# Kernel tuning notes

Hardware: AMD Instinct MI355X
Metric: run time of the kernel (lower is better)

Reference implementation:

```python
import jax, jax.numpy as jnp
import numpy as np

ALPHA = 0.2  # LeakyReLU negative slope

def setup_inputs() -> dict:
    key = jax.random.key(0)
    kx, kw, kb, ka = jax.random.split(key, 4)
    B, K, D, H = 4, 256, 128, 4
    x = jax.random.normal(kx, (B, K, D), dtype=jnp.float32)
    # Per-head Linear(2D -> D): stored as (H, 2D, D), i.e. transposed torch layout (y = v @ W + b)
    W = jax.random.normal(kw, (H, 2 * D, D), dtype=jnp.float32) * (1.0 / np.sqrt(2 * D))
    lin_b = jax.random.normal(kb, (H, D), dtype=jnp.float32) * 0.01
    # Per-head attention vector a: (H, D)
    a = jax.random.normal(ka, (H, D), dtype=jnp.float32) * (1.0 / np.sqrt(D))
    # Per-head additive bias over attention logits, initialized to zeros like the torch module
    bias = jnp.zeros((H, K, K), dtype=jnp.float32)
    return {"x": x, "W": W, "lin_b": lin_b, "a": a, "bias": bias}

def reference(x, W, lin_b, a, bias):
    # GATv2, dense all-pairs attention over K nodes, eval mode (dropout off).
    # Faithful decomposition: Linear(concat(x_i, x_j)) == x_i @ W_src + x_j @ W_dst + b
    B, K, D = x.shape
    H = W.shape[0]
    outs = []
    for h in range(H):  # small fixed head count; each head has distinct params
        W_src, W_dst = W[h, :D], W[h, D:]          # (D, D) each
        left = x @ W_src                            # (B, K, D) -> contribution of node i
        right = x @ W_dst                           # (B, K, D) -> contribution of node j
        s = left[:, :, None, :] + right[:, None, :, :] + lin_b[h]  # (B, K, K, D)
        s = jnp.where(s > 0, s, ALPHA * s)          # LeakyReLU
        e = jnp.einsum('bijd,d->bij', s, a[h]) + bias[h]           # (B, K, K)
        attn = jax.nn.softmax(e, axis=2)
        outs.append(attn @ x)                       # (B, K, D)
    return jnp.mean(jnp.stack(outs, axis=-1), axis=-1)
```

## Files before the change

### kernel.cpp

```cpp
#include <hip/hip_runtime.h>
#include <math.h>

constexpr int Kc = 256, Dc = 128, Mc = 1024;

typedef _Float16 h2_t __attribute__((ext_vector_type(2)));
union U32H2 { unsigned int u; h2_t h; };
__device__ inline h2_t u2h(unsigned int u) { U32H2 x; x.u = u; return x.h; }
__device__ inline unsigned int h2u(h2_t h) { U32H2 x; x.h = h; return x.u; }
__device__ inline unsigned int packh(float a, float b) {
    h2_t h; h.x = (_Float16)a; h.y = (_Float16)b; return h2u(h);
}

#if __has_builtin(__builtin_amdgcn_fdot2)
__device__ inline float dot2h(unsigned int a, unsigned int b, float c) {
    return __builtin_amdgcn_fdot2(u2h(a), u2h(b), c, false);
}
#else
__device__ inline float dot2h(unsigned int a, unsigned int b, float c) {
    h2_t ah = u2h(a), bh = u2h(b);
    return fmaf((float)ah.x, (float)bh.x, fmaf((float)ah.y, (float)bh.y, c));
}
#endif

__device__ inline float estep(unsigned int r, unsigned int l, h2_t av, float acc) {
    h2_t s = u2h(r) + u2h(l);
    unsigned int t = h2u(s) & 0x7FFF7FFFu;
#if __has_builtin(__builtin_amdgcn_fdot2)
    return __builtin_amdgcn_fdot2(u2h(t), av, acc, false);
#else
    h2_t th = u2h(t);
    return fmaf((float)th.x, (float)av.x, fmaf((float)th.y, (float)av.y, acc));
#endif
}

__global__ __launch_bounds__(512) void k1(const float* __restrict__ x,
                                          const float* __restrict__ W,
                                          const float* __restrict__ lin_b,
                                          const float* __restrict__ a,
                                          unsigned int* __restrict__ Lpp,
                                          unsigned int* __restrict__ Rtp,
                                          float* __restrict__ eb) {
    __shared__ unsigned int As2[64 * 64];
    __shared__ unsigned int Bs2[64 * 64];
    __shared__ float red[8][16][4];

    const int tid = threadIdx.x;
    const int bid = blockIdx.x;
    const int tx = tid & 15, ty = tid >> 4;
    const bool isL = (bid < 128);

    int h, b, m0, n0, dt;
    if (isL) {
        const int nt = bid & 1, mt = (bid >> 1) & 15;
        h = (bid >> 5) & 3; b = 0; dt = 0;
        m0 = mt * 64; n0 = nt * 64;
        {
            const int m_l = tid & 63, kq = tid >> 6;
            #pragma unroll
            for (int c = 0; c < 4; ++c) {
                const float4 v = *(const float4*)&x[(m0 + m_l) * Dc + kq * 16 + c * 4];
                As2[(kq * 8 + c * 2 + 0) * 64 + m_l] = packh(v.x, v.y);
                As2[(kq * 8 + c * 2 + 1) * 64 + m_l] = packh(v.z, v.w);
            }
        }
        {
            const int n_l = tid & 63, kq = tid >> 6;
            const float* Wb = W + (h * 2) * Dc * Dc;
            #pragma unroll
            for (int kk = 0; kk < 8; ++kk) {
                const int k2 = kq * 8 + kk;
                Bs2[k2 * 64 + n_l] =
                    packh(Wb[(2 * k2) * Dc + n0 + n_l], Wb[(2 * k2 + 1) * Dc + n0 + n_l]);
            }
        }
    } else {
        const int r_ = bid - 128;
        const int jt = r_ & 3;
        dt = (r_ >> 2) & 1;
        b  = (r_ >> 3) & 3;
        h  = (r_ >> 5) & 3;
        m0 = dt * 64;
        n0 = jt * 64;
        {
            const int d_l = tid & 63, kq = tid >> 6;
            const float* Wb = W + ((h * 2 + 1) * Dc) * Dc;
            #pragma unroll
            for (int kk = 0; kk < 8; ++kk) {
                const int k2 = kq * 8 + kk;
                As2[k2 * 64 + d_l] =
                    packh(Wb[(2 * k2) * Dc + m0 + d_l], Wb[(2 * k2 + 1) * Dc + m0 + d_l]);
            }
        }
        {
            const int j_l = tid & 63, kq = tid >> 6;
            #pragma unroll
            for (int c = 0; c < 4; ++c) {
                const float4 v = *(const float4*)&x[(b * Kc + n0 + j_l) * Dc + kq * 16 + c * 4];
                Bs2[(kq * 8 + c * 2 + 0) * 64 + j_l] = packh(v.x, v.y);
                Bs2[(kq * 8 + c * 2 + 1) * 64 + j_l] = packh(v.z, v.w);
            }
        }
    }
    __syncthreads();

    float acc[2][4];
    #pragma unroll
    for (int r = 0; r < 2; ++r)
        #pragma unroll
        for (int c = 0; c < 4; ++c) acc[r][c] = 0.f;

    #pragma unroll 8
    for (int k2 = 0; k2 < 64; ++k2) {
        const uint2 xa = *(const uint2*)&As2[k2 * 64 + ty * 2];
        const uint4 wb = *(const uint4*)&Bs2[k2 * 64 + tx * 4];
        acc[0][0] = dot2h(xa.x, wb.x, acc[0][0]);
        acc[0][1] = dot2h(xa.x, wb.y, acc[0][1]);
        acc[0][2] = dot2h(xa.x, wb.z, acc[0][2]);
        acc[0][3] = dot2h(xa.x, wb.w, acc[0][3]);
        acc[1][0] = dot2h(xa.y, wb.x, acc[1][0]);
        acc[1][1] = dot2h(xa.y, wb.y, acc[1][1]);
        acc[1][2] = dot2h(xa.y, wb.z, acc[1][2]);
        acc[1][3] = dot2h(xa.y, wb.w, acc[1][3]);
    }

    if (isL) {
        const float4 lv = *(const float4*)&lin_b[h * Dc + n0 + tx * 4];
        #pragma unroll
        for (int r = 0; r < 2; ++r) {
            uint2 pk;
            pk.x = packh(acc[r][0] + lv.x, acc[r][1] + lv.y);
            pk.y = packh(acc[r][2] + lv.z, acc[r][3] + lv.w);
            *(uint2*)&Lpp[(h * Mc + m0 + ty * 2 + r) * 64 + (n0 >> 1) + tx * 2] = pk;
        }
    } else {
        {
            uint4 pk;
            pk.x = packh(acc[0][0], acc[1][0]);
            pk.y = packh(acc[0][1], acc[1][1]);
            pk.z = packh(acc[0][2], acc[1][2]);
            pk.w = packh(acc[0][3], acc[1][3]);
            *(uint4*)&Rtp[((h * 4 + b) * 64 + (m0 >> 1) + ty) * Kc + n0 + tx * 4] = pk;
        }
        const float2 av = *(const float2*)&a[h * Dc + m0 + ty * 2];
        float p0 = 0.4f * (av.x * acc[0][0] + av.y * acc[1][0]);
        float p1 = 0.4f * (av.x * acc[0][1] + av.y * acc[1][1]);
        float p2 = 0.4f * (av.x * acc[0][2] + av.y * acc[1][2]);
        float p3 = 0.4f * (av.x * acc[0][3] + av.y * acc[1][3]);
        p0 += __shfl_xor(p0, 16, 64); p0 += __shfl_xor(p0, 32, 64);
        p1 += __shfl_xor(p1, 16, 64); p1 += __shfl_xor(p1, 32, 64);
        p2 += __shfl_xor(p2, 16, 64); p2 += __shfl_xor(p2, 32, 64);
        p3 += __shfl_xor(p3, 16, 64); p3 += __shfl_xor(p3, 32, 64);
        if (((tid >> 4) & 3) == 0) {
            const int w = tid >> 6;
            red[w][tx][0] = p0; red[w][tx][1] = p1;
            red[w][tx][2] = p2; red[w][tx][3] = p3;
        }
        __syncthreads();
        if (tid < 64) {
            const int txl = tid >> 2, c = tid & 3;
            float v = 0.f;
            #pragma unroll
            for (int w8 = 0; w8 < 8; ++w8) v += red[w8][txl][c];
            eb[((h * 4 + b) * 2 + dt) * Kc + n0 + tid] = 1.5f * v;
        }
    }
}

#define E4(ACC, LPV)                               \
    ACC.x = estep(rr.x, LPV, av, ACC.x);           \
    ACC.y = estep(rr.y, LPV, av, ACC.y);           \
    ACC.z = estep(rr.z, LPV, av, ACC.z);           \
    ACC.w = estep(rr.w, LPV, av, ACC.w);

__global__ __launch_bounds__(256) void k2(const float* __restrict__ x,
                                          const float* __restrict__ a,
                                          const float* __restrict__ bias,
                                          const unsigned int* __restrict__ Lpp,
                                          const unsigned int* __restrict__ Rtp,
                                          const float* __restrict__ eb,
                                          float* __restrict__ out) {
    __shared__ float red[256 * 12];
    __shared__ unsigned int lpT2[4 * 64 * 2];
    __shared__ unsigned int aa2s[4 * 64];
    __shared__ float plbar[2 * Kc];

    const int tid = threadIdx.x;
    const int L = blockIdx.x;
    const int xcd = L & 7;
    const int b = xcd >> 1;
    const int it = ((L >> 3) << 1) | (xcd & 1);
    const int i0 = it * 2;

    {
        const int hs = tid >> 6, dp = tid & 63;
        uint2 v;
        v.x = Lpp[(hs * Mc + b * Kc + i0 + 0) * 64 + dp];
        v.y = Lpp[(hs * Mc + b * Kc + i0 + 1) * 64 + dp];
        *(uint2*)&lpT2[(hs * 64 + dp) * 2] = v;
        aa2s[tid] = packh(0.4f * a[hs * Dc + 2 * dp], 0.4f * a[hs * Dc + 2 * dp + 1]);
    }
    __syncthreads();

    const int h = tid >> 6, j4 = tid & 63;
    const int hb = h * 4 + b;

    const float4 ebv0 = *(const float4*)&eb[(hb * 2 + 0) * Kc + j4 * 4];
    const float4 ebv1 = *(const float4*)&eb[(hb * 2 + 1) * Kc + j4 * 4];
    const float4 bv0  = *(const float4*)&bias[(h * Kc + i0 + 0) * Kc + j4 * 4];
    const float4 bv1  = *(const float4*)&bias[(h * Kc + i0 + 1) * Kc + j4 * 4];

    float4 acc0 = make_float4(0.f, 0.f, 0.f, 0.f);
    float4 acc1 = make_float4(0.f, 0.f, 0.f, 0.f);
    {
        const unsigned int* rb = Rtp + (hb * 64) * Kc + j4 * 4;
        const unsigned int* lt = lpT2 + (h * 64) * 2;
        const unsigned int* at = aa2s + h * 64;

        uint4 cur[8], nxt[8];
        #pragma unroll
        for (int i = 0; i < 8; ++i) cur[i] = *(const uint4*)(rb + i * Kc);

        #pragma unroll
        for (int bb = 0; bb < 8; ++bb) {
            #pragma unroll
            for (int i = 0; i < 8; ++i)
                if (bb < 7) nxt[i] = *(const uint4*)(rb + ((bb + 1) * 8 + i) * Kc);
            #pragma unroll
            for (int i = 0; i < 8; ++i) {
                const int dp = bb * 8 + i;
                const uint4 rr = cur[i];
                const uint2 lp2 = *(const uint2*)(lt + dp * 2);
                const h2_t av = u2h(at[dp]);
                E4(acc0, lp2.x);
                E4(acc1, lp2.y);
            }
            #pragma unroll
            for (int i = 0; i < 8; ++i)
                if (bb < 7) cur[i] = nxt[i];
        }
    }

    {
        const float jx = ebv0.x + ebv1.x, jy = ebv0.y + ebv1.y;
        const float jz = ebv0.z + ebv1.z, jw = ebv0.w + ebv1.w;
        acc0.x += jx + bv0.x; acc0.y += jy + bv0.y;
        acc0.z += jz + bv0.z; acc0.w += jw + bv0.w;
        acc1.x += jx + bv1.x; acc1.y += jy + bv1.y;
        acc1.z += jz + bv1.z; acc1.w += jw + bv1.w;

        {
            float m = fmaxf(fmaxf(acc0.x, acc0.y), fmaxf(acc0.z, acc0.w));
            #pragma unroll
            for (int off = 1; off < 64; off <<= 1) m = fmaxf(m, __shfl_xor(m, off, 64));
            const float p0 = __expf(acc0.x - m), p1 = __expf(acc0.y - m);
            const float p2 = __expf(acc0.z - m), p3 = __expf(acc0.w - m);
            float s = p0 + p1 + p2 + p3;
            #pragma unroll
            for (int off = 1; off < 64; off <<= 1) s += __shfl_xor(s, off, 64);
            const float sc = 0.25f / s;
            *(float4*)&red[h * 512 + 0 * Kc + j4 * 4] =
                make_float4(p0 * sc, p1 * sc, p2 * sc, p3 * sc);
        }
        {
            float m = fmaxf(fmaxf(acc1.x, acc1.y), fmaxf(acc1.z, acc1.w));
            #pragma unroll
            for (int off = 1; off < 64; off <<= 1) m = fmaxf(m, __shfl_xor(m, off, 64));
            const float p0 = __expf(acc1.x - m), p1 = __expf(acc1.y - m);
            const float p2 = __expf(acc1.z - m), p3 = __expf(acc1.w - m);
            float s = p0 + p1 + p2 + p3;
            #pragma unroll
            for (int off = 1; off < 64; off <<= 1) s += __shfl_xor(s, off, 64);
            const float sc = 0.25f / s;
            *(float4*)&red[h * 512 + 1 * Kc + j4 * 4] =
                make_float4(p0 * sc, p1 * sc, p2 * sc, p3 * sc);
        }
    }
    __syncthreads();

    if (tid < 128) {
        const int r = tid >> 6, c = tid & 63;
        float4 s = make_float4(0.f, 0.f, 0.f, 0.f);
        #pragma unroll
        for (int w4 = 0; w4 < 4; ++w4) {
            const float4 v = *(const float4*)&red[w4 * 512 + r * Kc + c * 4];
            s.x += v.x; s.y += v.y; s.z += v.z; s.w += v.w;
        }
        *(float4*)&plbar[r * Kc + c * 4] = s;
    }
    __syncthreads();

    const int jq = tid >> 5, dd4 = tid & 31;
    float4 o0 = make_float4(0.f, 0.f, 0.f, 0.f);
    float4 o1 = make_float4(0.f, 0.f, 0.f, 0.f);
    {
        const float* xb = x + (b * Kc) * Dc + dd4 * 4;
        float4 xc[8], xn[8];
        #pragma unroll
        for (int i = 0; i < 8; ++i) xc[i] = *(const float4*)(xb + (i * 8 + jq) * Dc);

        #pragma unroll
        for (int bb = 0; bb < 4; ++bb) {
            #pragma unroll
            for (int i = 0; i < 8; ++i)
                if (bb < 3) xn[i] = *(const float4*)(xb + (((bb + 1) * 8 + i) * 8 + jq) * Dc);
            #pragma unroll
            for (int i = 0; i < 8; ++i) {
                const int j = (bb * 8 + i) * 8 + jq;
                const float4 xv = xc[i];
                const float pv0 = plbar[j];
                const float pv1 = plbar[Kc + j];
                o0.x = fmaf(pv0, xv.x, o0.x); o0.y = fmaf(pv0, xv.y, o0.y);
                o0.z = fmaf(pv0, xv.z, o0.z); o0.w = fmaf(pv0, xv.w, o0.w);
                o1.x = fmaf(pv1, xv.x, o1.x); o1.y = fmaf(pv1, xv.y, o1.y);
                o1.z = fmaf(pv1, xv.z, o1.z); o1.w = fmaf(pv1, xv.w, o1.w);
            }
            #pragma unroll
            for (int i = 0; i < 8; ++i)
                if (bb < 3) xc[i] = xn[i];
        }
    }
    {
        float* myred = red + (jq * 32 + dd4) * 12;
        *(float4*)&myred[0] = o0;
        *(float4*)&myred[4] = o1;
    }
    __syncthreads();
    if (tid < 64) {
        const int i_f = tid >> 5, dd_f = tid & 31;
        float4 s = make_float4(0.f, 0.f, 0.f, 0.f);
        #pragma unroll
        for (int q = 0; q < 8; ++q) {
            const float4 v = *(const float4*)&red[(q * 32 + dd_f) * 12 + i_f * 4];
            s.x += v.x; s.y += v.y; s.z += v.z; s.w += v.w;
        }
        *(float4*)&out[(b * Kc + i0 + i_f) * Dc + dd_f * 4] = s;
    }
}

extern "C" void kernel_launch(void* const* d_in, const int* in_sizes, int n_in,
                              void* d_out, int out_size, void* d_ws, size_t ws_size,
                              hipStream_t stream) {
    const float* x     = (const float*)d_in[0];
    const float* W     = (const float*)d_in[1];
    const float* lin_b = (const float*)d_in[2];
    const float* a     = (const float*)d_in[3];
    const float* bias  = (const float*)d_in[4];
    float* out = (float*)d_out;

    unsigned int*   Lpp = (unsigned int*)d_ws;
    unsigned int*   Rtp = Lpp + 4 * Mc * 64;
    float*          eb  = (float*)(Rtp + 16 * 64 * Kc);

    k1<<<256, 512, 0, stream>>>(x, W, lin_b, a, Lpp, Rtp, eb);
    k2<<<512, 256, 0, stream>>>(x, a, bias, Lpp, Rtp, eb, out);
}
```

Before: 22.88 us.

## Process four query rows per k2 block with 512 threads to amortize x reads

Each k2 block now handles four query rows instead of two, using 512 threads (two waves per head), and the grid is halved to 256 blocks. The attention-weighted x aggregation reads each x row once for four output rows, halving global x traffic per output and amortizing setup and the a-vector packing. In exchange the block uses more shared memory (an extra pP buffer and a larger reduction buffer), has fewer blocks to fill the GPU, and the final reduction loop is longer.

```diff
diff --git a/kernel.cpp b/kernel.cpp
--- a/kernel.cpp
+++ b/kernel.cpp
@@ -172,48 +172,54 @@
     ACC.z = estep(rr.z, LPV, av, ACC.z);           \
     ACC.w = estep(rr.w, LPV, av, ACC.w);
 
-__global__ __launch_bounds__(256) void k2(const float* __restrict__ x,
+__global__ __launch_bounds__(512) void k2(const float* __restrict__ x,
                                           const float* __restrict__ a,
                                           const float* __restrict__ bias,
                                           const unsigned int* __restrict__ Lpp,
                                           const unsigned int* __restrict__ Rtp,
                                           const float* __restrict__ eb,
                                           float* __restrict__ out) {
-    __shared__ float red[256 * 12];
-    __shared__ unsigned int lpT2[4 * 64 * 2];
+    __shared__ float red[512 * 20];
+    __shared__ float pP[16 * Kc];
+    __shared__ unsigned int lpT2[4 * 64 * 4];
     __shared__ unsigned int aa2s[4 * 64];
-    __shared__ float plbar[2 * Kc];
+    __shared__ float plbar[4 * Kc];
 
     const int tid = threadIdx.x;
     const int L = blockIdx.x;
     const int xcd = L & 7;
     const int b = xcd >> 1;
     const int it = ((L >> 3) << 1) | (xcd & 1);
-    const int i0 = it * 2;
-
-    {
+    const int i0 = it * 4;
+
+    {
+        const int hs = tid >> 7, dp = tid & 63, ip = (tid >> 6) & 1;
+        uint2 v;
+        v.x = Lpp[(hs * Mc + b * Kc + i0 + ip * 2 + 0) * 64 + dp];
+        v.y = Lpp[(hs * Mc + b * Kc + i0 + ip * 2 + 1) * 64 + dp];
+        *(uint2*)&lpT2[(hs * 64 + dp) * 4 + ip * 2] = v;
+    }
+    if (tid < 256) {
         const int hs = tid >> 6, dp = tid & 63;
-        uint2 v;
-        v.x = Lpp[(hs * Mc + b * Kc + i0 + 0) * 64 + dp];
-        v.y = Lpp[(hs * Mc + b * Kc + i0 + 1) * 64 + dp];
-        *(uint2*)&lpT2[(hs * 64 + dp) * 2] = v;
         aa2s[tid] = packh(0.4f * a[hs * Dc + 2 * dp], 0.4f * a[hs * Dc + 2 * dp + 1]);
     }
     __syncthreads();
 
-    const int h = tid >> 6, j4 = tid & 63;
+    const int w = tid >> 6;
+    const int h = w >> 1, ih = w & 1, j4 = tid & 63;
     const int hb = h * 4 + b;
+    const int r0 = ih * 2, r1 = ih * 2 + 1;
 
     const float4 ebv0 = *(const float4*)&eb[(hb * 2 + 0) * Kc + j4 * 4];
     const float4 ebv1 = *(const float4*)&eb[(hb * 2 + 1) * Kc + j4 * 4];
-    const float4 bv0  = *(const float4*)&bias[(h * Kc + i0 + 0) * Kc + j4 * 4];
-    const float4 bv1  = *(const float4*)&bias[(h * Kc + i0 + 1) * Kc + j4 * 4];
+    const float4 bv0  = *(const float4*)&bias[(h * Kc + i0 + r0) * Kc + j4 * 4];
+    const float4 bv1  = *(const float4*)&bias[(h * Kc + i0 + r1) * Kc + j4 * 4];
 
     float4 acc0 = make_float4(0.f, 0.f, 0.f, 0.f);
     float4 acc1 = make_float4(0.f, 0.f, 0.f, 0.f);
     {
         const unsigned int* rb = Rtp + (hb * 64) * Kc + j4 * 4;
-        const unsigned int* lt = lpT2 + (h * 64) * 2;
+        const unsigned int* lt = lpT2 + (h * 64) * 4 + r0;
         const unsigned int* at = aa2s + h * 64;
 
         uint4 cur[8], nxt[8];
@@ -229,7 +235,7 @@
             for (int i = 0; i < 8; ++i) {
                 const int dp = bb * 8 + i;
                 const uint4 rr = cur[i];
-                const uint2 lp2 = *(const uint2*)(lt + dp * 2);
+                const uint2 lp2 = *(const uint2*)(lt + dp * 4);
                 const h2_t av = u2h(at[dp]);
                 E4(acc0, lp2.x);
                 E4(acc1, lp2.y);
@@ -258,7 +264,7 @@
             #pragma unroll
             for (int off = 1; off < 64; off <<= 1) s += __shfl_xor(s, off, 64);
             const float sc = 0.25f / s;
-            *(float4*)&red[h * 512 + 0 * Kc + j4 * 4] =
+            *(float4*)&pP[(h * 4 + r0) * Kc + j4 * 4] =
                 make_float4(p0 * sc, p1 * sc, p2 * sc, p3 * sc);
         }
         {
@@ -271,18 +277,18 @@
             #pragma unroll
             for (int off = 1; off < 64; off <<= 1) s += __shfl_xor(s, off, 64);
             const float sc = 0.25f / s;
-            *(float4*)&red[h * 512 + 1 * Kc + j4 * 4] =
+            *(float4*)&pP[(h * 4 + r1) * Kc + j4 * 4] =
                 make_float4(p0 * sc, p1 * sc, p2 * sc, p3 * sc);
         }
     }
     __syncthreads();
 
-    if (tid < 128) {
+    if (tid < 256) {
         const int r = tid >> 6, c = tid & 63;
         float4 s = make_float4(0.f, 0.f, 0.f, 0.f);
         #pragma unroll
-        for (int w4 = 0; w4 < 4; ++w4) {
-            const float4 v = *(const float4*)&red[w4 * 512 + r * Kc + c * 4];
+        for (int h4 = 0; h4 < 4; ++h4) {
+            const float4 v = *(const float4*)&pP[(h4 * 4 + r) * Kc + c * 4];
             s.x += v.x; s.y += v.y; s.z += v.z; s.w += v.w;
         }
         *(float4*)&plbar[r * Kc + c * 4] = s;
@@ -292,45 +298,55 @@
     const int jq = tid >> 5, dd4 = tid & 31;
     float4 o0 = make_float4(0.f, 0.f, 0.f, 0.f);
     float4 o1 = make_float4(0.f, 0.f, 0.f, 0.f);
+    float4 o2 = make_float4(0.f, 0.f, 0.f, 0.f);
+    float4 o3 = make_float4(0.f, 0.f, 0.f, 0.f);
     {
         const float* xb = x + (b * Kc) * Dc + dd4 * 4;
         float4 xc[8], xn[8];
         #pragma unroll
-        for (int i = 0; i < 8; ++i) xc[i] = *(const float4*)(xb + (i * 8 + jq) * Dc);
-
-        #pragma unroll
-        for (int bb = 0; bb < 4; ++bb) {
+        for (int i = 0; i < 8; ++i) xc[i] = *(const float4*)(xb + (i * 16 + jq) * Dc);
+
+        #pragma unroll
+        for (int bb = 0; bb < 2; ++bb) {
             #pragma unroll
             for (int i = 0; i < 8; ++i)
-                if (bb < 3) xn[i] = *(const float4*)(xb + (((bb + 1) * 8 + i) * 8 + jq) * Dc);
+                if (bb < 1) xn[i] = *(const float4*)(xb + (((bb + 1) * 8 + i) * 16 + jq) * Dc);
             #pragma unroll
             for (int i = 0; i < 8; ++i) {
-                const int j = (bb * 8 + i) * 8 + jq;
+                const int j = (bb * 8 + i) * 16 + jq;
                 const float4 xv = xc[i];
-                const float pv0 = plbar[j];
-                const float pv1 = plbar[Kc + j];
+                const float pv0 = plbar[0 * Kc + j];
+                const float pv1 = plbar[1 * Kc + j];
+                const float pv2 = plbar[2 * Kc + j];
+                const float pv3 = plbar[3 * Kc + j];
                 o0.x = fmaf(pv0, xv.x, o0.x); o0.y = fmaf(pv0, xv.y, o0.y);
                 o0.z = fmaf(pv0, xv.z, o0.z); o0.w = fmaf(pv0, xv.w, o0.w);
                 o1.x = fmaf(pv1, xv.x, o1.x); o1.y = fmaf(pv1, xv.y, o1.y);
                 o1.z = fmaf(pv1, xv.z, o1.z); o1.w = fmaf(pv1, xv.w, o1.w);
+                o2.x = fmaf(pv2, xv.x, o2.x); o2.y = fmaf(pv2, xv.y, o2.y);
+                o2.z = fmaf(pv2, xv.z, o2.z); o2.w = fmaf(pv2, xv.w, o2.w);
+                o3.x = fmaf(pv3, xv.x, o3.x); o3.y = fmaf(pv3, xv.y, o3.y);
+                o3.z = fmaf(pv3, xv.z, o3.z); o3.w = fmaf(pv3, xv.w, o3.w);
             }
             #pragma unroll
             for (int i = 0; i < 8; ++i)
-                if (bb < 3) xc[i] = xn[i];
-        }
-    }
-    {
-        float* myred = red + (jq * 32 + dd4) * 12;
-        *(float4*)&myred[0] = o0;
-        *(float4*)&myred[4] = o1;
-    }
-    __syncthreads();
-    if (tid < 64) {
+                if (bb < 1) xc[i] = xn[i];
+        }
+    }
+    {
+        float* myred = red + tid * 20;
+        *(float4*)&myred[0]  = o0;
+        *(float4*)&myred[4]  = o1;
+        *(float4*)&myred[8]  = o2;
+        *(float4*)&myred[12] = o3;
+    }
+    __syncthreads();
+    if (tid < 128) {
         const int i_f = tid >> 5, dd_f = tid & 31;
         float4 s = make_float4(0.f, 0.f, 0.f, 0.f);
         #pragma unroll
-        for (int q = 0; q < 8; ++q) {
-            const float4 v = *(const float4*)&red[(q * 32 + dd_f) * 12 + i_f * 4];
+        for (int q = 0; q < 16; ++q) {
+            const float4 v = *(const float4*)&red[(q * 32 + dd_f) * 20 + i_f * 4];
             s.x += v.x; s.y += v.y; s.z += v.z; s.w += v.w;
         }
         *(float4*)&out[(b * Kc + i0 + i_f) * Dc + dd_f * 4] = s;
@@ -352,5 +368,5 @@
     float*          eb  = (float*)(Rtp + 16 * 64 * Kc);
 
     k1<<<256, 512, 0, stream>>>(x, W, lin_b, a, Lpp, Rtp, eb);
-    k2<<<512, 256, 0, stream>>>(x, a, bias, Lpp, Rtp, eb, out);
-}
+    k2<<<256, 512, 0, stream>>>(x, a, bias, Lpp, Rtp, eb, out);
+}
```

Result: no change. 22.60 us (-1.2%).
